# Kernel tuning notes

Measured on AMD Instinct MI355X. Metric: run time of the kernel, lower is better.

## Reference

```python
import jax, jax.numpy as jnp
import numpy as np

INPUT_SIZE = 128
HIDDEN_SIZE = 128
OUTPUT_SIZE = 67  # hardcoded in the original module
SEQ_LEN = 512
BATCH = 2048


def setup_inputs() -> dict:
    key = jax.random.key(0)
    ks = jax.random.split(key, 7)
    x = jax.random.normal(ks[0], (INPUT_SIZE, SEQ_LEN, BATCH), dtype=jnp.float32)
    hidden = jax.random.normal(ks[1], (HIDDEN_SIZE, BATCH), dtype=jnp.float32)
    # bernoulli(0.5) mask applied column-wise to the initial hidden state
    drop_mask = jax.random.bernoulli(ks[2], 0.5, (HIDDEN_SIZE, BATCH)).astype(jnp.float32)
    # small init scale so tanh does not saturate
    Wi2h = jax.random.normal(ks[3], (HIDDEN_SIZE, INPUT_SIZE + HIDDEN_SIZE), dtype=jnp.float32) * 0.05
    bi2h = jax.random.normal(ks[4], (HIDDEN_SIZE,), dtype=jnp.float32) * 0.05
    Wi2o = jax.random.normal(ks[5], (OUTPUT_SIZE, HIDDEN_SIZE), dtype=jnp.float32) * 0.05
    bi2o = jax.random.normal(ks[6], (OUTPUT_SIZE,), dtype=jnp.float32) * 0.05
    return {"x": x, "hidden": hidden, "drop_mask": drop_mask,
            "Wi2h": Wi2h, "bi2h": bi2h, "Wi2o": Wi2o, "bi2o": bi2o}


def reference(x, hidden, drop_mask, Wi2h, bi2h, Wi2o, bi2o):
    # x: [input_size, seq_len, batch]; hidden: [hidden_size, batch]
    h0 = hidden * drop_mask  # per-column bernoulli dropout on initial state
    xs = jnp.transpose(x, (1, 0, 2))  # [seq, input_size, batch]

    def step(h, x_t):
        # combined = cat([x_t, h], dim=0).T -> [batch, input+hidden]
        combined = jnp.concatenate([x_t, h], axis=0).T
        h_new = jnp.tanh(combined @ Wi2h.T + bi2h)        # [batch, hidden]
        out = jax.nn.relu(h_new @ Wi2o.T + bi2o)          # [batch, output]
        return h_new.T, out.T                             # carry [hidden, batch], y [output, batch]

    _, ys = jax.lax.scan(step, h0, xs)  # ys: [seq, output, batch]
    Y = jnp.transpose(ys, (1, 0, 2))    # [output, seq, batch]
    return Y
```

## Files before the change

kernel.cpp:

```cpp
#include <hip/hip_runtime.h>
#include <hip/hip_bf16.h>
#include <stdint.h>

#define IN_SZ 128
#define HID 128
#define OUT_SZ 67
#define SEQ 512
#define BATCH 2048
#define BT 8
#define NTHR 384
#define SB (SEQ * BATCH)

typedef __attribute__((ext_vector_type(4))) float f32x4;
typedef __attribute__((ext_vector_type(8))) short s16x8;
typedef __attribute__((ext_vector_type(8))) __bf16 bf16x8;

static __device__ __forceinline__ unsigned short f2bf(float f) {
  union { float f; uint32_t u; } c; c.f = f;
  uint32_t u = c.u;
  uint32_t r = u + 0x7FFFu + ((u >> 16) & 1u);
  return (unsigned short)(r >> 16);
}
static __device__ __forceinline__ uint32_t pk2bf(float lo, float hi) {
  __hip_bfloat162 h2 = __float22bfloat162_rn(float2{lo, hi});
  union { __hip_bfloat162 h; uint32_t u; } c; c.h = h2;
  return c.u;
}
static __device__ __forceinline__ float fast_tanh(float x) {
  float e = __builtin_amdgcn_exp2f(x * 2.885390081777927f);
  float r = __builtin_amdgcn_rcpf(e + 1.f);
  return __builtin_fmaf(-2.f, r, 1.f);
}
static __device__ __forceinline__ void mfma16(f32x4& c, s16x8 a, s16x8 b) {
  c = __builtin_amdgcn_mfma_f32_16x16x32_bf16(
        __builtin_bit_cast(bf16x8, a), __builtin_bit_cast(bf16x8, b), c, 0, 0, 0);
}
#define KOFF(g, j) (4 * (g) + ((j) & 3) + (((j) >> 2) << 4))

static __device__ __forceinline__ void frag_barrier() {
  __builtin_amdgcn_sched_barrier(0);
  asm volatile("s_waitcnt lgkmcnt(0)");
  __builtin_amdgcn_s_barrier();
  __builtin_amdgcn_sched_barrier(0);
}

__global__ __launch_bounds__(NTHR, 1) void rnn_kernel(
    const float* __restrict__ x, const float* __restrict__ hidden,
    const float* __restrict__ mask, const float* __restrict__ Wi2h,
    const float* __restrict__ bi2h, const float* __restrict__ Wi2o,
    const float* __restrict__ bi2o, float* __restrict__ Y) {

  __shared__ s16x8 sX[3][4][64];
  __shared__ s16x8 sH[2][4][64];

  const int tid = threadIdx.x;
  const int wave = tid >> 6;
  const int lane = tid & 63;
  const int g = lane >> 4;
  const int n16 = lane & 15;
  const int bid = ((blockIdx.x & 7) << 5) | (blockIdx.x >> 3);
  const int b0 = bid * BT;

  if (wave < 4) {
    s16x8 W0[8], W1[8];
#pragma unroll
    for (int kt = 0; kt < 8; ++kt) {
      const float* wr0 = Wi2h + (size_t)(16 * (2 * wave + 0) + n16) * (IN_SZ + HID);
      const float* wr1 = Wi2h + (size_t)(16 * (2 * wave + 1) + n16) * (IN_SZ + HID);
      s16x8 w8a, w8b;
#pragma unroll
      for (int j = 0; j < 8; ++j) {
        w8a[j] = (short)f2bf(wr0[32 * kt + KOFF(g, j)]);
        w8b[j] = (short)f2bf(wr1[32 * kt + KOFF(g, j)]);
      }
      W0[kt] = w8a; W1[kt] = w8b;
    }
    f32x4 bhv0, bhv1;
#pragma unroll
    for (int r = 0; r < 4; ++r) {
      bhv0[r] = bi2h[16 * (2 * wave + 0) + 4 * g + r];
      bhv1[r] = bi2h[16 * (2 * wave + 1) + 4 * g + r];
    }

    const int nt = (wave == 3) ? 2 : 1;
    s16x8 wO[2][4];
    f32x4 bov[2];
    uint32_t ybase[2];
    int trow[2];
#pragma unroll
    for (int ot = 0; ot < 2; ++ot) {
      const int tk = (ot == 0) ? wave : 4;
      const bool tv = (ot < ((wave == 3) ? 2 : 1));
#pragma unroll
      for (int kk = 0; kk < 4; ++kk) {
        s16x8 a;
#pragma unroll
        for (int j = 0; j < 8; ++j) {
          int m = 16 * tk + n16;
          a[j] = (short)((tv && m < OUT_SZ)
                         ? f2bf(Wi2o[(size_t)m * HID + 32 * kk + KOFF(g, j)]) : 0);
        }
        wO[ot][kk] = a;
      }
#pragma unroll
      for (int r = 0; r < 4; ++r) {
        int m = 16 * tk + 4 * g + r;
        bov[ot][r] = (tv && m < OUT_SZ) ? bi2o[m] : 0.f;
      }
      ybase[ot] = (uint32_t)(16 * tk + 4 * g) * (uint32_t)SB + (uint32_t)(b0 + n16);
      trow[ot] = 16 * tk + 4 * g;
    }

    {
      const int cc = (b0 + n16 < BATCH) ? (b0 + n16) : (BATCH - 1);
      union { s16x8 v; uint32_t d[4]; } u;
#pragma unroll
      for (int q = 0; q < 4; ++q) {
        int r0 = 32 * wave + KOFF(g, 2 * q);
        int r1 = 32 * wave + KOFF(g, 2 * q + 1);
        float h0 = hidden[(size_t)r0 * BATCH + cc] * mask[(size_t)r0 * BATCH + cc];
        float h1 = hidden[(size_t)r1 * BATCH + cc] * mask[(size_t)r1 * BATCH + cc];
        u.d[q] = pk2bf(h0, h1);
      }
      sH[0][wave][lane] = u.v;
    }
    frag_barrier();

#define CSTEP(K)                                                                \
  {                                                                             \
    const int t = t6 + (K);                                                     \
    const int P = (K) & 1;                                                      \
    const int S = (K) % 3;                                                      \
    s16x8 X0 = sX[S][0][lane], X1 = sX[S][1][lane];                             \
    s16x8 X2 = sX[S][2][lane], X3 = sX[S][3][lane];                             \
    s16x8 H0 = sH[P][0][lane], H1 = sH[P][1][lane];                             \
    s16x8 H2 = sH[P][2][lane], H3 = sH[P][3][lane];                             \
    f32x4 a = bhv0, a2 = {0.f, 0.f, 0.f, 0.f};                                  \
    f32x4 b = bhv1, b2 = {0.f, 0.f, 0.f, 0.f};                                  \
    mfma16(a, W0[0], X0);  mfma16(a2, W0[1], X1);                               \
    mfma16(b, W1[0], X0);  mfma16(b2, W1[1], X1);                               \
    mfma16(a, W0[2], X2);  mfma16(a2, W0[3], X3);                               \
    mfma16(b, W1[2], X2);  mfma16(b2, W1[3], X3);                               \
    mfma16(a, W0[4], H0);  mfma16(a2, W0[5], H1);                               \
    mfma16(b, W1[4], H0);  mfma16(b2, W1[5], H1);                               \
    mfma16(a, W0[6], H2);  mfma16(a2, W0[7], H3);                               \
    mfma16(b, W1[6], H2);  mfma16(b2, W1[7], H3);                               \
             \
    {                                                                           \
      f32x4 s0 = a + a2, s1 = b + b2;                                           \
      union { s16x8 v; uint32_t d[4]; } u;                                      \
      u.d[0] = pk2bf(fast_tanh(s0[0]), fast_tanh(s0[1]));                       \
      u.d[1] = pk2bf(fast_tanh(s0[2]), fast_tanh(s0[3]));                       \
      u.d[2] = pk2bf(fast_tanh(s1[0]), fast_tanh(s1[1]));                       \
      u.d[3] = pk2bf(fast_tanh(s1[2]), fast_tanh(s1[3]));                       \
      sH[P ^ 1][wave][lane] = u.v;                                              \
    }                                                                           \
      \
    if (t > 0) {                                                                \
      const uint32_t ty = (uint32_t)(t - 1) * (uint32_t)BATCH;                  \
      _Pragma("unroll")                                                         \
      for (int ot = 0; ot < 2; ++ot) {                                          \
        if (ot < nt) {                                                          \
          f32x4 ao = bov[ot];                                                   \
          mfma16(ao, wO[ot][0], H0); mfma16(ao, wO[ot][1], H1);                 \
          mfma16(ao, wO[ot][2], H2); mfma16(ao, wO[ot][3], H3);                 \
          if (n16 < BT) {                                                       \
            _Pragma("unroll")                                                   \
            for (int r = 0; r < 4; ++r)                                         \
              if (trow[ot] + r < OUT_SZ)                                        \
                Y[(size_t)(ybase[ot] + (uint32_t)r * SB + ty)] = fmaxf(ao[r], 0.f); \
          }                                                                     \
        }                                                                       \
      }                                                                         \
    }                                                                           \
    frag_barrier();                                                             \
  }

    for (int t6 = 0; t6 < 510; t6 += 6) {
      CSTEP(0) CSTEP(1) CSTEP(2) CSTEP(3) CSTEP(4) CSTEP(5)
    }
    {
      const int t6 = 510;
      CSTEP(0) CSTEP(1)
    }
#undef CSTEP

    {
      s16x8 H0 = sH[0][0][lane], H1 = sH[0][1][lane];
      s16x8 H2 = sH[0][2][lane], H3 = sH[0][3][lane];
      const uint32_t ty = 511u * (uint32_t)BATCH;
#pragma unroll
      for (int ot = 0; ot < 2; ++ot) {
        if (ot < nt) {
          f32x4 ao = bov[ot];
          mfma16(ao, wO[ot][0], H0); mfma16(ao, wO[ot][1], H1);
          mfma16(ao, wO[ot][2], H2); mfma16(ao, wO[ot][3], H3);
          if (n16 < BT) {
#pragma unroll
            for (int r = 0; r < 4; ++r)
              if (trow[ot] + r < OUT_SZ)
                Y[(size_t)(ybase[ot] + (uint32_t)r * SB + ty)] = fmaxf(ao[r], 0.f);
          }
        }
      }
    }

  } else {
    const int svl = ((wave - 4) << 6) | lane;
    const int rp = svl >> 1;
    const int R0 = 2 * rp;
    const int lcb = (svl & 1) * 4;
    const int skk = R0 >> 5;
    const int r5 = R0 & 31;
    const int sg = (r5 < 16) ? (r5 >> 2) : ((r5 - 16) >> 2);
    const int sq = ((r5 & 2) >> 1) + ((r5 < 16) ? 0 : 2);
    const int slb = sg << 4;
    const char* const xB = (const char*)x;
    const uint32_t xr0 = ((uint32_t)R0 * (uint32_t)SB + (uint32_t)b0) * 4u;
    const uint32_t xr1 = ((uint32_t)(R0 + 1) * (uint32_t)SB + (uint32_t)b0) * 4u;

#pragma unroll
    for (int tt = 0; tt < 2; ++tt) {
      const uint32_t to = (uint32_t)tt * (BATCH * 4u);
#pragma unroll
      for (int i = 0; i < 4; ++i) {
        const int lc = lcb + i;
        float v0 = *(const float*)(xB + xr0 + to + 4u * lc);
        float v1 = *(const float*)(xB + xr1 + to + 4u * lc);
        ((uint32_t*)&sX[tt][skk][slb | lc])[sq] = pk2bf(v0, v1);
      }
    }
    float q0[8], q1[8], q2[8], q3[8], q4[8], q5[8];
#define FILLQ(Q, T)                                                             \
    {                                                                           \
      const uint32_t to = (uint32_t)(T) * (BATCH * 4u);                         \
      _Pragma("unroll")                                                         \
      for (int i = 0; i < 4; ++i) {                                             \
        Q[2 * i]     = *(const float*)(xB + xr0 + to + 4u * (lcb + i));         \
        Q[2 * i + 1] = *(const float*)(xB + xr1 + to + 4u * (lcb + i));         \
      }                                                                         \
    }
    FILLQ(q0, 2) FILLQ(q1, 3) FILLQ(q2, 4) FILLQ(q3, 5) FILLQ(q4, 6) FILLQ(q5, 7)
    frag_barrier();

#define SSTEP(K, Q)                                                             \
  {                                                                             \
    const int t = t6 + (K);                                                     \
    const int SW = ((K) + 2) % 3;                                               \
    _Pragma("unroll")                                                           \
    for (int i = 0; i < 4; ++i) {                                               \
      const int lc = lcb + i;                                                   \
      ((uint32_t*)&sX[SW][skk][slb | lc])[sq] = pk2bf(Q[2 * i], Q[2 * i + 1]);  \
    }                                                                           \
    {                                                                           \
      const int tn = (t + 8 > 511) ? 511 : t + 8;                               \
      FILLQ(Q, tn)                                                              \
    }                                                                           \
    frag_barrier();                                                             \
  }

    for (int t6 = 0; t6 < 510; t6 += 6) {
      SSTEP(0, q0) SSTEP(1, q1) SSTEP(2, q2) SSTEP(3, q3) SSTEP(4, q4) SSTEP(5, q5)
    }
    {
      const int t6 = 510;
      SSTEP(0, q0) SSTEP(1, q1)
    }
#undef SSTEP
#undef FILLQ
  }
}

extern "C" void kernel_launch(void* const* d_in, const int* in_sizes, int n_in,
                              void* d_out, int out_size, void* d_ws, size_t ws_size,
                              hipStream_t stream) {
  const float* x      = (const float*)d_in[0];
  const float* hidden = (const float*)d_in[1];
  const float* mask   = (const float*)d_in[2];
  const float* Wi2h   = (const float*)d_in[3];
  const float* bi2h   = (const float*)d_in[4];
  const float* Wi2o   = (const float*)d_in[5];
  const float* bi2o   = (const float*)d_in[6];
  float* Y = (float*)d_out;
  (void)in_sizes; (void)n_in; (void)out_size; (void)d_ws; (void)ws_size;
  rnn_kernel<<<dim3(BATCH / BT), dim3(NTHR), 0, stream>>>(
      x, hidden, mask, Wi2h, bi2h, Wi2o, bi2o, Y);
}
```

Measured before the change: 434.3 us.

## Move input projection to producer waves and pass preactivations through LDS

Moves the input projection x_t·Wi2h_x + bias off the serial critical path. The two producer waves now compute it one step ahead with MFMA and write fp32 preactivations to shared memory, so the consumer waves only do the hidden-to-hidden MFMAs, tanh and the output projection each step. Each producer wave now loads x directly in MFMA fragment layout and keeps its own x-weight slice in registers, with a 3-deep prefetch ring in place of the previous 6. The trade-off is more register use and LDS traffic in the producer waves, and the producers' longer per-step work could become the new bottleneck.

```diff
diff --git a/kernel.cpp b/kernel.cpp
--- a/kernel.cpp
+++ b/kernel.cpp
@@ -50,8 +50,8 @@
     const float* __restrict__ bi2h, const float* __restrict__ Wi2o,
     const float* __restrict__ bi2o, float* __restrict__ Y) {
 
-  __shared__ s16x8 sX[3][4][64];
   __shared__ s16x8 sH[2][4][64];
+  __shared__ f32x4 sA[2][8][64];
 
   const int tid = threadIdx.x;
   const int wave = tid >> 6;
@@ -60,26 +60,21 @@
   const int n16 = lane & 15;
   const int bid = ((blockIdx.x & 7) << 5) | (blockIdx.x >> 3);
   const int b0 = bid * BT;
+  const int cc = (b0 + n16 < BATCH) ? (b0 + n16) : (BATCH - 1);
 
   if (wave < 4) {
-    s16x8 W0[8], W1[8];
-#pragma unroll
-    for (int kt = 0; kt < 8; ++kt) {
+    s16x8 WH0[4], WH1[4];
+#pragma unroll
+    for (int kk = 0; kk < 4; ++kk) {
       const float* wr0 = Wi2h + (size_t)(16 * (2 * wave + 0) + n16) * (IN_SZ + HID);
       const float* wr1 = Wi2h + (size_t)(16 * (2 * wave + 1) + n16) * (IN_SZ + HID);
-      s16x8 w8a, w8b;
+      s16x8 a, b;
 #pragma unroll
       for (int j = 0; j < 8; ++j) {
-        w8a[j] = (short)f2bf(wr0[32 * kt + KOFF(g, j)]);
-        w8b[j] = (short)f2bf(wr1[32 * kt + KOFF(g, j)]);
-      }
-      W0[kt] = w8a; W1[kt] = w8b;
-    }
-    f32x4 bhv0, bhv1;
-#pragma unroll
-    for (int r = 0; r < 4; ++r) {
-      bhv0[r] = bi2h[16 * (2 * wave + 0) + 4 * g + r];
-      bhv1[r] = bi2h[16 * (2 * wave + 1) + 4 * g + r];
+        a[j] = (short)f2bf(wr0[IN_SZ + 32 * kk + KOFF(g, j)]);
+        b[j] = (short)f2bf(wr1[IN_SZ + 32 * kk + KOFF(g, j)]);
+      }
+      WH0[kk] = a; WH1[kk] = b;
     }
 
     const int nt = (wave == 3) ? 2 : 1;
@@ -90,7 +85,7 @@
 #pragma unroll
     for (int ot = 0; ot < 2; ++ot) {
       const int tk = (ot == 0) ? wave : 4;
-      const bool tv = (ot < ((wave == 3) ? 2 : 1));
+      const bool tv = (ot < nt);
 #pragma unroll
       for (int kk = 0; kk < 4; ++kk) {
         s16x8 a;
@@ -112,7 +107,6 @@
     }
 
     {
-      const int cc = (b0 + n16 < BATCH) ? (b0 + n16) : (BATCH - 1);
       union { s16x8 v; uint32_t d[4]; } u;
 #pragma unroll
       for (int q = 0; q < 4; ++q) {
@@ -130,21 +124,15 @@
   {                                                                             \
     const int t = t6 + (K);                                                     \
     const int P = (K) & 1;                                                      \
-    const int S = (K) % 3;                                                      \
-    s16x8 X0 = sX[S][0][lane], X1 = sX[S][1][lane];                             \
-    s16x8 X2 = sX[S][2][lane], X3 = sX[S][3][lane];                             \
+    f32x4 a = sA[P][2 * wave + 0][lane];                  \
+    f32x4 b = sA[P][2 * wave + 1][lane];                                        \
     s16x8 H0 = sH[P][0][lane], H1 = sH[P][1][lane];                             \
     s16x8 H2 = sH[P][2][lane], H3 = sH[P][3][lane];                             \
-    f32x4 a = bhv0, a2 = {0.f, 0.f, 0.f, 0.f};                                  \
-    f32x4 b = bhv1, b2 = {0.f, 0.f, 0.f, 0.f};                                  \
-    mfma16(a, W0[0], X0);  mfma16(a2, W0[1], X1);                               \
-    mfma16(b, W1[0], X0);  mfma16(b2, W1[1], X1);                               \
-    mfma16(a, W0[2], X2);  mfma16(a2, W0[3], X3);                               \
-    mfma16(b, W1[2], X2);  mfma16(b2, W1[3], X3);                               \
-    mfma16(a, W0[4], H0);  mfma16(a2, W0[5], H1);                               \
-    mfma16(b, W1[4], H0);  mfma16(b2, W1[5], H1);                               \
-    mfma16(a, W0[6], H2);  mfma16(a2, W0[7], H3);                               \
-    mfma16(b, W1[6], H2);  mfma16(b2, W1[7], H3);                               \
+    f32x4 a2 = {0.f, 0.f, 0.f, 0.f}, b2 = {0.f, 0.f, 0.f, 0.f};                 \
+    mfma16(a, WH0[0], H0);  mfma16(a2, WH0[1], H1);                             \
+    mfma16(b, WH1[0], H0);  mfma16(b2, WH1[1], H1);                             \
+    mfma16(a, WH0[2], H2);  mfma16(a2, WH0[3], H3);                             \
+    mfma16(b, WH1[2], H2);  mfma16(b2, WH1[3], H3);                             \
              \
     {                                                                           \
       f32x4 s0 = a + a2, s1 = b + b2;                                           \
@@ -155,7 +143,7 @@
       u.d[3] = pk2bf(fast_tanh(s1[2]), fast_tanh(s1[3]));                       \
       sH[P ^ 1][wave][lane] = u.v;                                              \
     }                                                                           \
-      \
+                         \
     if (t > 0) {                                                                \
       const uint32_t ty = (uint32_t)(t - 1) * (uint32_t)BATCH;                  \
       _Pragma("unroll")                                                         \
@@ -206,67 +194,96 @@
     }
 
   } else {
-    const int svl = ((wave - 4) << 6) | lane;
-    const int rp = svl >> 1;
-    const int R0 = 2 * rp;
-    const int lcb = (svl & 1) * 4;
-    const int skk = R0 >> 5;
-    const int r5 = R0 & 31;
-    const int sg = (r5 < 16) ? (r5 >> 2) : ((r5 - 16) >> 2);
-    const int sq = ((r5 & 2) >> 1) + ((r5 < 16) ? 0 : 2);
-    const int slb = sg << 4;
+    const int sv = wave - 4;
+    const int tb = 4 * sv;
+
+    s16x8 Wx[4][4];
+    f32x4 bhv4[4];
+#pragma unroll
+    for (int tt = 0; tt < 4; ++tt) {
+      const float* wr = Wi2h + (size_t)(16 * (tb + tt) + n16) * (IN_SZ + HID);
+#pragma unroll
+      for (int kk = 0; kk < 4; ++kk) {
+        s16x8 a;
+#pragma unroll
+        for (int j = 0; j < 8; ++j)
+          a[j] = (short)f2bf(wr[32 * kk + KOFF(g, j)]);
+        Wx[tt][kk] = a;
+      }
+#pragma unroll
+      for (int r = 0; r < 4; ++r)
+        bhv4[tt][r] = bi2h[16 * (tb + tt) + 4 * g + r];
+    }
+
     const char* const xB = (const char*)x;
-    const uint32_t xr0 = ((uint32_t)R0 * (uint32_t)SB + (uint32_t)b0) * 4u;
-    const uint32_t xr1 = ((uint32_t)(R0 + 1) * (uint32_t)SB + (uint32_t)b0) * 4u;
-
-#pragma unroll
-    for (int tt = 0; tt < 2; ++tt) {
-      const uint32_t to = (uint32_t)tt * (BATCH * 4u);
-#pragma unroll
-      for (int i = 0; i < 4; ++i) {
-        const int lc = lcb + i;
-        float v0 = *(const float*)(xB + xr0 + to + 4u * lc);
-        float v1 = *(const float*)(xB + xr1 + to + 4u * lc);
-        ((uint32_t*)&sX[tt][skk][slb | lc])[sq] = pk2bf(v0, v1);
-      }
-    }
-    float q0[8], q1[8], q2[8], q3[8], q4[8], q5[8];
+    uint32_t xo[8];
+#pragma unroll
+    for (int j = 0; j < 8; ++j)
+      xo[j] = ((uint32_t)KOFF(g, j) * (uint32_t)SB + (uint32_t)cc) * 4u;
+    const uint32_t KSTRIDE = 32u * (uint32_t)SB * 4u;
+
 #define FILLQ(Q, T)                                                             \
     {                                                                           \
-      const uint32_t to = (uint32_t)(T) * (BATCH * 4u);                         \
+      const uint32_t to = (uint32_t)(T) * ((uint32_t)BATCH * 4u);               \
       _Pragma("unroll")                                                         \
-      for (int i = 0; i < 4; ++i) {                                             \
-        Q[2 * i]     = *(const float*)(xB + xr0 + to + 4u * (lcb + i));         \
-        Q[2 * i + 1] = *(const float*)(xB + xr1 + to + 4u * (lcb + i));         \
+      for (int kk = 0; kk < 4; ++kk)                                            \
+        _Pragma("unroll")                                                       \
+        for (int j = 0; j < 8; ++j)                                             \
+          Q[8 * kk + j] = *(const float*)(xB + xo[j] + kk * KSTRIDE + to);      \
+    }
+#define AXCOMP(Q, DST)                                                          \
+    {                                                                           \
+      s16x8 X0, X1, X2, X3;                                                     \
+      {                                                                         \
+        union { s16x8 v; uint32_t d[4]; } u;                                    \
+        _Pragma("unroll")                                                       \
+        for (int q = 0; q < 4; ++q) u.d[q] = pk2bf(Q[2 * q], Q[2 * q + 1]);     \
+        X0 = u.v;                                                               \
+        _Pragma("unroll")                                                       \
+        for (int q = 0; q < 4; ++q) u.d[q] = pk2bf(Q[8 + 2 * q], Q[9 + 2 * q]); \
+        X1 = u.v;                                                               \
+        _Pragma("unroll")                                                       \
+        for (int q = 0; q < 4; ++q) u.d[q] = pk2bf(Q[16 + 2 * q], Q[17 + 2 * q]); \
+        X2 = u.v;                                                               \
+        _Pragma("unroll")                                                       \
+        for (int q = 0; q < 4; ++q) u.d[q] = pk2bf(Q[24 + 2 * q], Q[25 + 2 * q]); \
+        X3 = u.v;                                                               \
       }                                                                         \
-    }
-    FILLQ(q0, 2) FILLQ(q1, 3) FILLQ(q2, 4) FILLQ(q3, 5) FILLQ(q4, 6) FILLQ(q5, 7)
+      _Pragma("unroll")                                                         \
+      for (int tt = 0; tt < 4; ++tt) {                                          \
+        f32x4 ac = bhv4[tt];                                                    \
+        mfma16(ac, Wx[tt][0], X0); mfma16(ac, Wx[tt][1], X1);                   \
+        mfma16(ac, Wx[tt][2], X2); mfma16(ac, Wx[tt][3], X3);                   \
+        sA[DST][tb + tt][lane] = ac;                                            \
+      }                                                                         \
+    }
+
+    float q0[32], q1[32], q2[32];
+    FILLQ(q0, 0)
+    AXCOMP(q0, 0)
+    FILLQ(q0, 1) FILLQ(q1, 2) FILLQ(q2, 3)
     frag_barrier();
 
 #define SSTEP(K, Q)                                                             \
   {                                                                             \
     const int t = t6 + (K);                                                     \
-    const int SW = ((K) + 2) % 3;                                               \
-    _Pragma("unroll")                                                           \
-    for (int i = 0; i < 4; ++i) {                                               \
-      const int lc = lcb + i;                                                   \
-      ((uint32_t*)&sX[SW][skk][slb | lc])[sq] = pk2bf(Q[2 * i], Q[2 * i + 1]);  \
-    }                                                                           \
+    AXCOMP(Q, ((K) & 1) ^ 1)                                                    \
     {                                                                           \
-      const int tn = (t + 8 > 511) ? 511 : t + 8;                               \
+      const int tn = (t + 4 > 511) ? 511 : t + 4;                               \
       FILLQ(Q, tn)                                                              \
     }                                                                           \
     frag_barrier();                                                             \
   }
 
     for (int t6 = 0; t6 < 510; t6 += 6) {
-      SSTEP(0, q0) SSTEP(1, q1) SSTEP(2, q2) SSTEP(3, q3) SSTEP(4, q4) SSTEP(5, q5)
+      SSTEP(0, q0) SSTEP(1, q1) SSTEP(2, q2) SSTEP(3, q0) SSTEP(4, q1) SSTEP(5, q2)
     }
     {
       const int t6 = 510;
       SSTEP(0, q0) SSTEP(1, q1)
     }
 #undef SSTEP
+#undef AXCOMP
 #undef FILLQ
   }
 }
```

After: 641.1 us. 1.48x slower.

## Move output projection to a dedicated seventh wave off the recurrence path

Applied to the files above, without the earlier changes.

The four compute waves previously ran both the hidden-state recurrence and the output projection (Wi2o MFMAs plus Y stores), with wave 3 handling two output tiles. This adds a seventh wave that does all five output tiles from the shared hidden buffer, one step behind, so the recurrence waves only do the Wi2h MFMAs and tanh. The goal is to shorten the serial per-step critical path. In exchange the block grows to 448 threads, and the new wave's five-tile chain of 20 MFMAs plus stores per step must keep pace between barriers, or it becomes the new bottleneck.

```diff
diff --git a/kernel.cpp b/kernel.cpp
--- a/kernel.cpp
+++ b/kernel.cpp
@@ -8,7 +8,7 @@
 #define SEQ 512
 #define BATCH 2048
 #define BT 8
-#define NTHR 384
+#define NTHR 448
 #define SB (SEQ * BATCH)
 
 typedef __attribute__((ext_vector_type(4))) float f32x4;
@@ -60,6 +60,7 @@
   const int n16 = lane & 15;
   const int bid = ((blockIdx.x & 7) << 5) | (blockIdx.x >> 3);
   const int b0 = bid * BT;
+  const int cc = (b0 + n16 < BATCH) ? (b0 + n16) : (BATCH - 1);
 
   if (wave < 4) {
     s16x8 W0[8], W1[8];
@@ -82,37 +83,7 @@
       bhv1[r] = bi2h[16 * (2 * wave + 1) + 4 * g + r];
     }
 
-    const int nt = (wave == 3) ? 2 : 1;
-    s16x8 wO[2][4];
-    f32x4 bov[2];
-    uint32_t ybase[2];
-    int trow[2];
-#pragma unroll
-    for (int ot = 0; ot < 2; ++ot) {
-      const int tk = (ot == 0) ? wave : 4;
-      const bool tv = (ot < ((wave == 3) ? 2 : 1));
-#pragma unroll
-      for (int kk = 0; kk < 4; ++kk) {
-        s16x8 a;
-#pragma unroll
-        for (int j = 0; j < 8; ++j) {
-          int m = 16 * tk + n16;
-          a[j] = (short)((tv && m < OUT_SZ)
-                         ? f2bf(Wi2o[(size_t)m * HID + 32 * kk + KOFF(g, j)]) : 0);
-        }
-        wO[ot][kk] = a;
-      }
-#pragma unroll
-      for (int r = 0; r < 4; ++r) {
-        int m = 16 * tk + 4 * g + r;
-        bov[ot][r] = (tv && m < OUT_SZ) ? bi2o[m] : 0.f;
-      }
-      ybase[ot] = (uint32_t)(16 * tk + 4 * g) * (uint32_t)SB + (uint32_t)(b0 + n16);
-      trow[ot] = 16 * tk + 4 * g;
-    }
-
     {
-      const int cc = (b0 + n16 < BATCH) ? (b0 + n16) : (BATCH - 1);
       union { s16x8 v; uint32_t d[4]; } u;
 #pragma unroll
       for (int q = 0; q < 4; ++q) {
@@ -128,7 +99,6 @@
 
 #define CSTEP(K)                                                                \
   {                                                                             \
-    const int t = t6 + (K);                                                     \
     const int P = (K) & 1;                                                      \
     const int S = (K) % 3;                                                      \
     s16x8 X0 = sX[S][0][lane], X1 = sX[S][1][lane];                             \
@@ -145,7 +115,6 @@
     mfma16(b, W1[4], H0);  mfma16(b2, W1[5], H1);                               \
     mfma16(a, W0[6], H2);  mfma16(a2, W0[7], H3);                               \
     mfma16(b, W1[6], H2);  mfma16(b2, W1[7], H3);                               \
-             \
     {                                                                           \
       f32x4 s0 = a + a2, s1 = b + b2;                                           \
       union { s16x8 v; uint32_t d[4]; } u;                                      \
@@ -155,57 +124,16 @@
       u.d[3] = pk2bf(fast_tanh(s1[2]), fast_tanh(s1[3]));                       \
       sH[P ^ 1][wave][lane] = u.v;                                              \
     }                                                                           \
-      \
-    if (t > 0) {                                                                \
-      const uint32_t ty = (uint32_t)(t - 1) * (uint32_t)BATCH;                  \
-      _Pragma("unroll")                                                         \
-      for (int ot = 0; ot < 2; ++ot) {                                          \
-        if (ot < nt) {                                                          \
-          f32x4 ao = bov[ot];                                                   \
-          mfma16(ao, wO[ot][0], H0); mfma16(ao, wO[ot][1], H1);                 \
-          mfma16(ao, wO[ot][2], H2); mfma16(ao, wO[ot][3], H3);                 \
-          if (n16 < BT) {                                                       \
-            _Pragma("unroll")                                                   \
-            for (int r = 0; r < 4; ++r)                                         \
-              if (trow[ot] + r < OUT_SZ)                                        \
-                Y[(size_t)(ybase[ot] + (uint32_t)r * SB + ty)] = fmaxf(ao[r], 0.f); \
-          }                                                                     \
-        }                                                                       \
-      }                                                                         \
-    }                                                                           \
     frag_barrier();                                                             \
   }
 
     for (int t6 = 0; t6 < 510; t6 += 6) {
       CSTEP(0) CSTEP(1) CSTEP(2) CSTEP(3) CSTEP(4) CSTEP(5)
     }
-    {
-      const int t6 = 510;
-      CSTEP(0) CSTEP(1)
-    }
+    CSTEP(0) CSTEP(1)
 #undef CSTEP
 
-    {
-      s16x8 H0 = sH[0][0][lane], H1 = sH[0][1][lane];
-      s16x8 H2 = sH[0][2][lane], H3 = sH[0][3][lane];
-      const uint32_t ty = 511u * (uint32_t)BATCH;
-#pragma unroll
-      for (int ot = 0; ot < 2; ++ot) {
-        if (ot < nt) {
-          f32x4 ao = bov[ot];
-          mfma16(ao, wO[ot][0], H0); mfma16(ao, wO[ot][1], H1);
-          mfma16(ao, wO[ot][2], H2); mfma16(ao, wO[ot][3], H3);
-          if (n16 < BT) {
-#pragma unroll
-            for (int r = 0; r < 4; ++r)
-              if (trow[ot] + r < OUT_SZ)
-                Y[(size_t)(ybase[ot] + (uint32_t)r * SB + ty)] = fmaxf(ao[r], 0.f);
-          }
-        }
-      }
-    }
-
-  } else {
+  } else if (wave < 6) {
     const int svl = ((wave - 4) << 6) | lane;
     const int rp = svl >> 1;
     const int R0 = 2 * rp;
@@ -268,6 +196,73 @@
     }
 #undef SSTEP
 #undef FILLQ
+
+  } else {
+    s16x8 wO[5][4];
+    f32x4 bov[5];
+    uint32_t ybase[5];
+    int trow[5];
+#pragma unroll
+    for (int ot = 0; ot < 5; ++ot) {
+#pragma unroll
+      for (int kk = 0; kk < 4; ++kk) {
+        s16x8 a;
+#pragma unroll
+        for (int j = 0; j < 8; ++j) {
+          int m = 16 * ot + n16;
+          a[j] = (short)((m < OUT_SZ)
+                         ? f2bf(Wi2o[(size_t)m * HID + 32 * kk + KOFF(g, j)]) : 0);
+        }
+        wO[ot][kk] = a;
+      }
+#pragma unroll
+      for (int r = 0; r < 4; ++r) {
+        int m = 16 * ot + 4 * g + r;
+        bov[ot][r] = (m < OUT_SZ) ? bi2o[m] : 0.f;
+      }
+      ybase[ot] = (uint32_t)(16 * ot + 4 * g) * (uint32_t)SB + (uint32_t)(b0 + n16);
+      trow[ot] = 16 * ot + 4 * g;
+    }
+
+    frag_barrier();
+    frag_barrier();
+
+    for (int t = 1; t < SEQ; ++t) {
+      const int P = t & 1;
+      s16x8 H0 = sH[P][0][lane], H1 = sH[P][1][lane];
+      s16x8 H2 = sH[P][2][lane], H3 = sH[P][3][lane];
+      const uint32_t ty = (uint32_t)(t - 1) * (uint32_t)BATCH;
+#pragma unroll
+      for (int ot = 0; ot < 5; ++ot) {
+        f32x4 ao = bov[ot];
+        mfma16(ao, wO[ot][0], H0); mfma16(ao, wO[ot][1], H1);
+        mfma16(ao, wO[ot][2], H2); mfma16(ao, wO[ot][3], H3);
+        if (n16 < BT) {
+#pragma unroll
+          for (int r = 0; r < 4; ++r)
+            if (trow[ot] + r < OUT_SZ)
+              Y[(size_t)(ybase[ot] + (uint32_t)r * SB + ty)] = fmaxf(ao[r], 0.f);
+        }
+      }
+      frag_barrier();
+    }
+    {
+      s16x8 H0 = sH[0][0][lane], H1 = sH[0][1][lane];
+      s16x8 H2 = sH[0][2][lane], H3 = sH[0][3][lane];
+      const uint32_t ty = 511u * (uint32_t)BATCH;
+#pragma unroll
+      for (int ot = 0; ot < 5; ++ot) {
+        f32x4 ao = bov[ot];
+        mfma16(ao, wO[ot][0], H0); mfma16(ao, wO[ot][1], H1);
+        mfma16(ao, wO[ot][2], H2); mfma16(ao, wO[ot][3], H3);
+        if (n16 < BT) {
+#pragma unroll
+          for (int r = 0; r < 4; ++r)
+            if (trow[ot] + r < OUT_SZ)
+              Y[(size_t)(ybase[ot] + (uint32_t)r * SB + ty)] = fmaxf(ao[r], 0.f);
+        }
+      }
+    }
   }
 }
 
```

Measured after the change: 431.8 us. About the same (-0.6%).
